# Kernel optimization log

Measured on AMD Instinct MI355X. Metric: run time of the kernel, lower is better.

## Reference

```python
import jax, jax.numpy as jnp
import numpy as np

B, N, D_MODEL, H, DK, DV = 2, 2048, 512, 8, 64, 64


def setup_inputs() -> dict:
    key = jax.random.key(0)
    ks = jax.random.split(key, 15)
    s = 0.02
    f = jnp.float32
    inp = {
        "x": jax.random.normal(ks[0], (B, N, D_MODEL), f),
        # frozen base projections
        "Wq": jax.random.normal(ks[1], (D_MODEL, H * DK), f) * s,
        "bq": jax.random.normal(ks[2], (H * DK,), f) * s,
        "Wk": jax.random.normal(ks[3], (D_MODEL, H * DK), f) * s,
        "bk": jax.random.normal(ks[4], (H * DK,), f) * s,
        "Wv": jax.random.normal(ks[5], (D_MODEL, H * DV), f) * s,
        "bv": jax.random.normal(ks[6], (H * DV,), f) * s,
        # 'lora' adapters (full linears in the source, added to base)
        "Wq_lora": jax.random.normal(ks[7], (D_MODEL, H * DK), f) * s,
        "bq_lora": jax.random.normal(ks[8], (H * DK,), f) * s,
        "Wk_lora": jax.random.normal(ks[9], (D_MODEL, H * DK), f) * s,
        "bk_lora": jax.random.normal(ks[10], (H * DK,), f) * s,
        "Wv_lora": jax.random.normal(ks[11], (D_MODEL, H * DV), f) * s,
        "bv_lora": jax.random.normal(ks[12], (H * DV,), f) * s,
        # output projection
        "Wo": jax.random.normal(ks[13], (H * DV, D_MODEL), f) * s,
        "bo": jax.random.normal(ks[14], (D_MODEL,), f) * s,
    }
    return inp


def reference(x, Wq, bq, Wk, bk, Wv, bv,
              Wq_lora, bq_lora, Wk_lora, bk_lora, Wv_lora, bv_lora,
              Wo, bo):
    b, n, _ = x.shape
    # base + lora pairs share the same input -> fuse into single GEMMs
    q = x @ (Wq + Wq_lora) + (bq + bq_lora)          # [b, n, H*DK]
    k = x @ (Wk + Wk_lora) + (bk + bk_lora)          # [b, n, H*DK]
    v = x @ (Wv + Wv_lora) + (bv + bv_lora)          # [b, n, H*DV]

    q = q.reshape(b, n, H, DK).transpose(0, 2, 1, 3)  # [b, H, n, DK]
    k = k.reshape(b, n, H, DK).transpose(0, 2, 1, 3)
    v = v.reshape(b, n, H, DV).transpose(0, 2, 1, 3)

    scale = 1.0 / jnp.sqrt(jnp.asarray(DK, x.dtype))
    scores = jnp.einsum('bhqd,bhkd->bhqk', q, k) * scale  # [b, H, n, n]
    att = jax.nn.softmax(scores, axis=-1)                 # attn dropout = eval identity
    out = jnp.einsum('bhqk,bhkd->bhqd', att, v)           # [b, H, n, DV]
    out = out.transpose(0, 2, 1, 3).reshape(b, n, H * DV)
    return out @ Wo + bo                                  # resid dropout = eval identity
```

## Files before the change

kernel.cpp:

```cpp
#include <hip/hip_runtime.h>
#include <hip/hip_bf16.h>

#define B_  2
#define N_  2048
#define DM_ 512
#define H_  8
#define DK_ 64
#define DV_ 64
#define BN_ (B_*N_)
#define SPLITS 2

typedef __attribute__((ext_vector_type(8))) short short8;
typedef __attribute__((ext_vector_type(4))) float f32x4;
typedef unsigned short ushort;
typedef __attribute__((address_space(3))) unsigned int lds_u32_t;
typedef const __attribute__((address_space(1))) unsigned int glb_u32_t;

static __device__ __forceinline__ ushort f2bf(float x) {
    unsigned int u = __float_as_uint(x);
    unsigned int r = (u + 0x7FFFu + ((u >> 16) & 1u)) >> 16;
    return (ushort)r;
}
static __device__ __forceinline__ float bf2f(ushort u) {
    return __uint_as_float(((unsigned)u) << 16);
}
static __device__ __forceinline__ float exp2_fast(float x) {
    float r; asm("v_exp_f32 %0, %1" : "=v"(r) : "v"(x)); return r;
}
static __device__ __forceinline__ unsigned cvt_pk_bf16(float a, float b) {
    unsigned r; asm("v_cvt_pk_bf16_f32 %0, %1, %2" : "=v"(r) : "v"(a), "v"(b)); return r;
}

#define LOG2E 1.4426950408889634f

__global__ __launch_bounds__(256) void prep(
        const float* __restrict__ W0, const float* __restrict__ L0,
        const float* __restrict__ W1, const float* __restrict__ L1,
        const float* __restrict__ W2, const float* __restrict__ L2,
        const float* __restrict__ W3, ushort* __restrict__ WtBase,
        const float* __restrict__ x, ushort* __restrict__ xb,
        const float* __restrict__ bq, const float* __restrict__ bqL,
        const float* __restrict__ bk, const float* __restrict__ bkL,
        const float* __restrict__ bv, const float* __restrict__ bvL,
        float* __restrict__ fb) {
    const int bid = blockIdx.x;
    const int t = threadIdx.x;
    if (bid < 512) {
        const int z = bid >> 7, rem = bid & 127;
        const int c0 = (rem & 7) * 64, k0 = (rem >> 3) * 32;
        const float* W  = (z == 0) ? W0 : (z == 1) ? W1 : (z == 2) ? W2 : W3;
        const float* WL = (z == 0) ? L0 : (z == 1) ? L1 : (z == 2) ? L2 : nullptr;
        ushort* Wt = WtBase + (size_t)z * DM_ * DM_;
        __shared__ float Ws[32][65];
        {
            int r = t >> 4, cq = t & 15;
#pragma unroll
            for (int it = 0; it < 2; ++it) {
                int rr = r + it * 16;
                float4 v = *reinterpret_cast<const float4*>(W + (size_t)(k0 + rr) * DM_ + c0 + cq * 4);
                if (WL) {
                    float4 u = *reinterpret_cast<const float4*>(WL + (size_t)(k0 + rr) * DM_ + c0 + cq * 4);
                    v.x += u.x; v.y += u.y; v.z += u.z; v.w += u.w;
                }
                Ws[rr][cq * 4 + 0] = v.x; Ws[rr][cq * 4 + 1] = v.y;
                Ws[rr][cq * 4 + 2] = v.z; Ws[rr][cq * 4 + 3] = v.w;
            }
        }
        __syncthreads();
        {
            int cr = t >> 2, kq = t & 3;
            short8 o;
#pragma unroll
            for (int j = 0; j < 8; ++j) o[j] = (short)f2bf(Ws[kq * 8 + j][cr]);
            *reinterpret_cast<short8*>(Wt + (size_t)(c0 + cr) * DM_ + k0 + kq * 8) = o;
        }
    } else if (bid < 1536) {
        size_t idx = (size_t)(bid - 512) * 256 + t;
        float4 v0 = *reinterpret_cast<const float4*>(x + idx * 8);
        float4 v1 = *reinterpret_cast<const float4*>(x + idx * 8 + 4);
        short8 o;
        o[0] = (short)f2bf(v0.x); o[1] = (short)f2bf(v0.y);
        o[2] = (short)f2bf(v0.z); o[3] = (short)f2bf(v0.w);
        o[4] = (short)f2bf(v1.x); o[5] = (short)f2bf(v1.y);
        o[6] = (short)f2bf(v1.z); o[7] = (short)f2bf(v1.w);
        *reinterpret_cast<short8*>(xb + idx * 8) = o;
    } else {
        int idx = (bid - 1536) * 256 + t;
        if (idx < 3 * DM_) {
            int w = idx >> 9, i = idx & 511;
            const float* a = (w == 0) ? bq : (w == 1) ? bk : bv;
            const float* b = (w == 0) ? bqL : (w == 1) ? bkL : bvL;
            fb[idx] = a[i] + b[i];
        }
    }
}

template<int BN, int MODE>
__global__ __launch_bounds__(256) void gemm_bf16(const ushort* __restrict__ A,
                                                 const ushort* __restrict__ Bt,
                                                 const float* __restrict__ bias,
                                                 ushort* __restrict__ Qd,
                                                 ushort* __restrict__ Kd,
                                                 ushort* __restrict__ Vd,
                                                 float* __restrict__ outF) {
    constexpr int NWC = BN / 64;
    constexpr int NWR = 4 / NWC;
    constexpr int MI  = (128 / NWR) / 16;
    constexpr int NJ  = 4;
    constexpr int BIT = BN / 32;
    const int rt = blockIdx.x, ct = blockIdx.y;
    __shared__ ushort As[2][128 * 64];
    __shared__ ushort Bs[2][BN * 64];
    const int t = threadIdx.x, lane = t & 63, w = t >> 6;
    const int wr = w / NWC, wc = w % NWC;
    const int lg = lane >> 4, lr = lane & 15;
    const int rowbase = wr * (128 / NWR);
    const int colbase = wc * 64;

    f32x4 acc[MI][NJ];
#pragma unroll
    for (int mi = 0; mi < MI; ++mi)
#pragma unroll
        for (int nj = 0; nj < NJ; ++nj) acc[mi][nj] = (f32x4){0.f, 0.f, 0.f, 0.f};

    auto stage = [&](int buf, int k0) {
#pragma unroll
        for (int it = 0; it < 4; ++it) {
            int c = it * 256 + t;
            int r = c >> 3, cq = c & 7;
            int gq = cq ^ (r & 7);
            __builtin_amdgcn_global_load_lds(
                (glb_u32_t*)(A + ((size_t)(rt * 128 + r)) * DM_ + k0 + gq * 8),
                (lds_u32_t*)((char*)(As[buf]) + c * 16), 16, 0, 0);
        }
#pragma unroll
        for (int it = 0; it < BIT; ++it) {
            int c = it * 256 + t;
            int r = c >> 3, cq = c & 7;
            int gq = cq ^ (r & 7);
            __builtin_amdgcn_global_load_lds(
                (glb_u32_t*)(Bt + ((size_t)(ct * BN + r)) * DM_ + k0 + gq * 8),
                (lds_u32_t*)((char*)(Bs[buf]) + c * 16), 16, 0, 0);
        }
    };

    stage(0, 0);
    __syncthreads();

    for (int k0 = 0; k0 < DM_; k0 += 64) {
        const int cur = (k0 >> 6) & 1;
        if (k0 + 64 < DM_) stage(cur ^ 1, k0 + 64);
#pragma unroll
        for (int kh = 0; kh < 2; ++kh) {
            short8 a[MI], b[NJ];
#pragma unroll
            for (int mi = 0; mi < MI; ++mi) {
                int row = rowbase + mi * 16 + lr;
                a[mi] = *reinterpret_cast<const short8*>(
                    (char*)(As[cur]) + row * 128 + (((kh * 4 + lg) ^ (row & 7)) << 4));
            }
#pragma unroll
            for (int nj = 0; nj < NJ; ++nj) {
                int row = colbase + nj * 16 + lr;
                b[nj] = *reinterpret_cast<const short8*>(
                    (char*)(Bs[cur]) + row * 128 + (((kh * 4 + lg) ^ (row & 7)) << 4));
            }
#pragma unroll
            for (int mi = 0; mi < MI; ++mi)
#pragma unroll
                for (int nj = 0; nj < NJ; ++nj)
                    acc[mi][nj] = __builtin_amdgcn_mfma_f32_16x16x32_bf16(
                        a[mi], b[nj], acc[mi][nj], 0, 0, 0);
        }
        __syncthreads();
    }

#pragma unroll
    for (int mi = 0; mi < MI; ++mi) {
#pragma unroll
        for (int nj = 0; nj < NJ; ++nj) {
#pragma unroll
            for (int r = 0; r < 4; ++r) {
                int m = rt * 128 + rowbase + mi * 16 + 4 * lg + r;
                int n = ct * BN + colbase + nj * 16 + lr;
                float v = acc[mi][nj][r] + bias[n];
                if (MODE == 0) {
                    int ws_ = n >> 9;
                    if (ws_ == 0) v *= 0.125f * LOG2E;
                    ushort* op = (ws_ == 0) ? Qd : (ws_ == 1) ? Kd : Vd;
                    int hd = (n >> 6) & 7, d = n & 63;
                    int bb = m >> 11, nn = m & (N_ - 1);
                    op[(((size_t)(bb * H_ + hd)) * N_ + nn) * DK_ + d] = f2bf(v);
                } else {
                    outF[(size_t)m * DM_ + n] = v;
                }
            }
        }
    }
}

__global__ __launch_bounds__(256) void vtrans(const ushort* __restrict__ Vd,
                                              ushort* __restrict__ Vt) {
    const int bh = blockIdx.y, nt = blockIdx.x;
    __shared__ ushort Ls[64 * 64];
    char* LB = (char*)Ls;
    const int t = threadIdx.x;
#pragma unroll
    for (int i = 0; i < 2; ++i) {
        int c = t + i * 256;
        int tok = c >> 3, dc = c & 7;
        uint4 v = *reinterpret_cast<const uint4*>(
            Vd + ((size_t)bh * N_ + nt * 64 + tok) * DV_ + dc * 8);
        int sw = dc ^ (tok & 7) ^ ((tok >> 3) & 7);
        *reinterpret_cast<uint4*>(LB + tok * 128 + (sw << 4)) = v;
    }
    __syncthreads();
#pragma unroll
    for (int i = 0; i < 2; ++i) {
        int c = t + i * 256;
        int d = c >> 3, tc = c & 7;
        short8 g;
#pragma unroll
        for (int j = 0; j < 8; ++j) {
            int tok = tc * 8 + j;
            int sw = (d >> 3) ^ (tok & 7) ^ ((tok >> 3) & 7);
            g[j] = *reinterpret_cast<const ushort*>(LB + tok * 128 + (sw << 4) + (d & 7) * 2);
        }
        *reinterpret_cast<short8*>(Vt + ((size_t)bh * DV_ + d) * N_ + nt * 64 + tc * 8) = g;
    }
}

__global__ __launch_bounds__(512) void attn_mfma(const ushort* __restrict__ Q,
                                                 const ushort* __restrict__ K,
                                                 const ushort* __restrict__ Vt,
                                                 ushort* __restrict__ Opart,
                                                 float2* __restrict__ Ml) {
    const int bh = blockIdx.y;
    const int qt = blockIdx.x;
    const int sp = blockIdx.z;
    const int t  = threadIdx.x;
    const int lane = t & 63;
    const int w  = t >> 6;
    const int lg = lane >> 4;
    const int lr = lane & 15;

    __shared__ ushort KsBuf[2][64 * 64];
    __shared__ ushort VtBuf[2][64 * 64];
    __shared__ ushort Ps[8][16 * 64];
    char* PsB = (char*)(Ps[w]);

    const ushort* Kb  = K  + ((size_t)bh * N_ + sp * (N_ / 2)) * DK_;
    const ushort* Vtb = Vt + (size_t)bh * DV_ * N_ + sp * (N_ / 2);

    const int srow = t >> 3, sc = t & 7;

    short8 qf[2];
    {
        const ushort* qrow = Q + ((size_t)bh * N_ + qt * 128 + w * 16 + lr) * DK_;
        qf[0] = *reinterpret_cast<const short8*>(qrow + 8 * lg);
        qf[1] = *reinterpret_cast<const short8*>(qrow + 32 + 8 * lg);
    }

    f32x4 o_[4];
#pragma unroll
    for (int i = 0; i < 4; i++) o_[i] = (f32x4){0.f, 0.f, 0.f, 0.f};
    float m1 = -1e30f, l1 = 0.f;

    uint4 kreg, vreg;
    auto issue = [&](int kt_) {
        kreg = *reinterpret_cast<const uint4*>(Kb  + ((size_t)(kt_ * 64 + srow)) * DK_ + sc * 8);
        vreg = *reinterpret_cast<const uint4*>(Vtb + (size_t)srow * N_ + kt_ * 64 + sc * 8);
    };
    auto wstage = [&](int buf_) {
        *reinterpret_cast<uint4*>((char*)(KsBuf[buf_]) + srow * 128 + ((sc ^ (srow & 7)) << 4)) = kreg;
        *reinterpret_cast<uint4*>((char*)(VtBuf[buf_]) + srow * 128 + ((sc ^ (srow & 7)) << 4)) = vreg;
    };

    issue(0);
    wstage(0);
    __syncthreads();

    const int NT = (N_ / 2) / 64;
    for (int kt = 0; kt < NT; ++kt) {
        const int cur = kt & 1;
        if (kt + 1 < NT) issue(kt + 1);

        char* KsB = (char*)(KsBuf[cur]);
        char* VtB = (char*)(VtBuf[cur]);

        f32x4 s[4];
#pragma unroll
        for (int kb = 0; kb < 4; ++kb) {
            int row = kb * 16 + lr;
            short8 k0 = *reinterpret_cast<const short8*>(
                KsB + row * 128 + ((lg ^ (row & 7)) << 4));
            short8 k1 = *reinterpret_cast<const short8*>(
                KsB + row * 128 + (((4 + lg) ^ (row & 7)) << 4));
            f32x4 z = (f32x4){0.f, 0.f, 0.f, 0.f};
            s[kb] = __builtin_amdgcn_mfma_f32_16x16x32_bf16(k0, qf[0], z, 0, 0, 0);
            s[kb] = __builtin_amdgcn_mfma_f32_16x16x32_bf16(k1, qf[1], s[kb], 0, 0, 0);
        }

        float mx = s[0][0];
#pragma unroll
        for (int kb = 0; kb < 4; ++kb)
#pragma unroll
            for (int r = 0; r < 4; ++r) mx = fmaxf(mx, s[kb][r]);
        mx = fmaxf(mx, __shfl_xor(mx, 16));
        mx = fmaxf(mx, __shfl_xor(mx, 32));

        if (!__all(mx <= m1 + 8.0f)) {
            float mnew = fmaxf(m1, mx);
            float alpha = exp2_fast(m1 - mnew);
            m1 = mnew;
            l1 *= alpha;
#pragma unroll
            for (int r = 0; r < 4; ++r) {
                float ar = __shfl(alpha, 4 * lg + r);
#pragma unroll
                for (int db = 0; db < 4; ++db) o_[db][r] *= ar;
            }
        }

        float p[4][4];
        float sum = 0.f;
#pragma unroll
        for (int kb = 0; kb < 4; ++kb)
#pragma unroll
            for (int r = 0; r < 4; ++r) { p[kb][r] = exp2_fast(s[kb][r] - m1); sum += p[kb][r]; }
        sum += __shfl_xor(sum, 16);
        sum += __shfl_xor(sum, 32);
        l1 += sum;

#pragma unroll
        for (int kb = 0; kb < 4; ++kb) {
            uint2 pk;
            pk.x = cvt_pk_bf16(p[kb][0], p[kb][1]);
            pk.y = cvt_pk_bf16(p[kb][2], p[kb][3]);
            int chunk = 2 * kb + (lg >> 1);
            *reinterpret_cast<uint2*>(
                PsB + lr * 128 + ((chunk ^ (lr & 7)) << 4) + (lg & 1) * 8) = pk;
        }

        short8 pf[2];
        {
            pf[0] = *reinterpret_cast<const short8*>(
                PsB + lr * 128 + ((lg ^ (lr & 7)) << 4));
            pf[1] = *reinterpret_cast<const short8*>(
                PsB + lr * 128 + (((4 + lg) ^ (lr & 7)) << 4));
        }
#pragma unroll
        for (int db = 0; db < 4; ++db) {
            int row = db * 16 + lr;
            short8 v0 = *reinterpret_cast<const short8*>(
                VtB + row * 128 + ((lg ^ (row & 7)) << 4));
            short8 v1 = *reinterpret_cast<const short8*>(
                VtB + row * 128 + (((4 + lg) ^ (row & 7)) << 4));
            o_[db] = __builtin_amdgcn_mfma_f32_16x16x32_bf16(pf[0], v0, o_[db], 0, 0, 0);
            o_[db] = __builtin_amdgcn_mfma_f32_16x16x32_bf16(pf[1], v1, o_[db], 0, 0, 0);
        }

        if (kt + 1 < NT) wstage(cur ^ 1);
        __syncthreads();
    }

    const size_t rowbase = ((size_t)(sp * 16 + bh)) * N_ + qt * 128 + w * 16;
#pragma unroll
    for (int r = 0; r < 4; ++r) {
        int n_loc = 4 * lg + r;
#pragma unroll
        for (int db = 0; db < 4; ++db) {
            Opart[(rowbase + n_loc) * DV_ + db * 16 + lr] = f2bf(o_[db][r]);
        }
    }
    if (lg == 0) {
        Ml[rowbase + lr] = make_float2(m1, l1);
    }
}

__global__ __launch_bounds__(256) void merge_splits(const ushort* __restrict__ Opart,
                                                    const float2* __restrict__ Ml,
                                                    ushort* __restrict__ Od) {
    int gid = blockIdx.x * 256 + threadIdx.x;
    int row = gid >> 4;
    int dv  = (gid & 15) * 4;
    const int R = 16 * N_;
    float2 ml0 = Ml[row];
    float2 ml1 = Ml[R + row];
    float M  = fmaxf(ml0.x, ml1.x);
    float w0 = exp2_fast(ml0.x - M);
    float w1 = exp2_fast(ml1.x - M);
    float inv = 1.f / (w0 * ml0.y + w1 * ml1.y);
    uint2 a = *reinterpret_cast<const uint2*>(Opart + (size_t)row * DV_ + dv);
    uint2 b = *reinterpret_cast<const uint2*>(Opart + ((size_t)R + row) * DV_ + dv);
    const ushort* ae = reinterpret_cast<const ushort*>(&a);
    const ushort* be = reinterpret_cast<const ushort*>(&b);
    uint2 o;
    unsigned* oe = reinterpret_cast<unsigned*>(&o);
#pragma unroll
    for (int half = 0; half < 2; ++half) {
        float v0 = (w0 * bf2f(ae[half * 2 + 0]) + w1 * bf2f(be[half * 2 + 0])) * inv;
        float v1 = (w0 * bf2f(ae[half * 2 + 1]) + w1 * bf2f(be[half * 2 + 1])) * inv;
        oe[half] = cvt_pk_bf16(v0, v1);
    }
    int bh = row >> 11, n = row & (N_ - 1);
    int bb = bh >> 3, h = bh & 7;
    *reinterpret_cast<uint2*>(Od + ((size_t)(bb * N_ + n)) * (H_ * DV_) + h * DV_ + dv) = o;
}

extern "C" void kernel_launch(void* const* d_in, const int* in_sizes, int n_in,
                              void* d_out, int out_size, void* d_ws, size_t ws_size,
                              hipStream_t stream) {
    const float* x   = (const float*)d_in[0];
    const float* Wq  = (const float*)d_in[1];
    const float* bq  = (const float*)d_in[2];
    const float* Wk  = (const float*)d_in[3];
    const float* bk  = (const float*)d_in[4];
    const float* Wv  = (const float*)d_in[5];
    const float* bv  = (const float*)d_in[6];
    const float* WqL = (const float*)d_in[7];
    const float* bqL = (const float*)d_in[8];
    const float* WkL = (const float*)d_in[9];
    const float* bkL = (const float*)d_in[10];
    const float* WvL = (const float*)d_in[11];
    const float* bvL = (const float*)d_in[12];
    const float* Wo  = (const float*)d_in[13];
    const float* bo  = (const float*)d_in[14];

    ushort* Wt_all = (ushort*)d_ws;
    ushort* Wot    = Wt_all + (size_t)3 * DM_ * DM_;
    float*  fb     = (float*)(Wt_all + (size_t)4 * DM_ * DM_);
    ushort* xbf    = (ushort*)(fb + 3 * DM_);
    ushort* Qd     = xbf + (size_t)BN_ * DM_;
    ushort* Kd     = Qd + (size_t)B_ * H_ * N_ * DK_;
    ushort* Vd     = Kd + (size_t)B_ * H_ * N_ * DK_;
    ushort* Vtd    = Vd + (size_t)B_ * H_ * N_ * DV_;
    ushort* Od     = Vtd + (size_t)B_ * H_ * N_ * DV_;
    ushort* Opart  = Od + (size_t)B_ * H_ * N_ * DV_;
    float2* Ml     = (float2*)(Opart + (size_t)SPLITS * B_ * H_ * N_ * DV_);

    float* out = (float*)d_out;

    prep<<<1542, 256, 0, stream>>>(Wq, WqL, Wk, WkL, Wv, WvL, Wo, Wt_all,
                                   x, xbf, bq, bqL, bk, bkL, bv, bvL, fb);

    gemm_bf16<128, 0><<<dim3(32, 12), 256, 0, stream>>>(xbf, Wt_all, fb, Qd, Kd, Vd, nullptr);
    vtrans<<<dim3(32, 16), 256, 0, stream>>>(Vd, Vtd);
    attn_mfma<<<dim3(16, 16, SPLITS), 512, 0, stream>>>(Qd, Kd, Vtd, Opart, Ml);
    merge_splits<<<(B_ * H_ * N_ * 16) / 256, 256, 0, stream>>>(Opart, Ml, Od);
    gemm_bf16<64, 1><<<dim3(32, 8), 256, 0, stream>>>(Od, Wot, bo, nullptr, nullptr, nullptr, out);
}
```

Measured before the change: 72.28 us.

## Fuse V transpose into QKV GEMM epilogue and raise attention splits to four

The QKV GEMM epilogue now writes V straight into the transposed [bh, d, n] layout as packed bf16 quads, so the separate vtrans kernel and the intermediate V buffer are gone. Attention splits along the key dimension go from 2 to 4, doubling the attention grid to 1024 blocks for better CU occupancy, and merge_splits is generalised to combine any number of partials. The cost is twice as much partial-output and max/sum traffic plus a heavier merge, and the transposed V stores from the GEMM are 8-byte scattered writes.

```diff
diff --git a/kernel.cpp b/kernel.cpp
--- a/kernel.cpp
+++ b/kernel.cpp
@@ -8,7 +8,7 @@
 #define DK_ 64
 #define DV_ 64
 #define BN_ (B_*N_)
-#define SPLITS 2
+#define SPLITS 4
 
 typedef __attribute__((ext_vector_type(8))) short short8;
 typedef __attribute__((ext_vector_type(4))) float f32x4;
@@ -101,7 +101,7 @@
                                                  const float* __restrict__ bias,
                                                  ushort* __restrict__ Qd,
                                                  ushort* __restrict__ Kd,
-                                                 ushort* __restrict__ Vd,
+                                                 ushort* __restrict__ Vtd,
                                                  float* __restrict__ outF) {
     constexpr int NWC = BN / 64;
     constexpr int NWR = 4 / NWC;
@@ -179,54 +179,37 @@
     for (int mi = 0; mi < MI; ++mi) {
 #pragma unroll
         for (int nj = 0; nj < NJ; ++nj) {
-#pragma unroll
-            for (int r = 0; r < 4; ++r) {
-                int m = rt * 128 + rowbase + mi * 16 + 4 * lg + r;
-                int n = ct * BN + colbase + nj * 16 + lr;
-                float v = acc[mi][nj][r] + bias[n];
-                if (MODE == 0) {
-                    int ws_ = n >> 9;
+            int n = ct * BN + colbase + nj * 16 + lr;
+            int m0 = rt * 128 + rowbase + mi * 16 + 4 * lg;
+            if (MODE == 1) {
+#pragma unroll
+                for (int r = 0; r < 4; ++r)
+                    outF[(size_t)(m0 + r) * DM_ + n] = acc[mi][nj][r] + bias[n];
+            } else {
+                int ws_ = n >> 9;
+                float vv[4];
+#pragma unroll
+                for (int r = 0; r < 4; ++r) {
+                    float v = acc[mi][nj][r] + bias[n];
                     if (ws_ == 0) v *= 0.125f * LOG2E;
-                    ushort* op = (ws_ == 0) ? Qd : (ws_ == 1) ? Kd : Vd;
-                    int hd = (n >> 6) & 7, d = n & 63;
-                    int bb = m >> 11, nn = m & (N_ - 1);
-                    op[(((size_t)(bb * H_ + hd)) * N_ + nn) * DK_ + d] = f2bf(v);
+                    vv[r] = v;
+                }
+                int hd = (n >> 6) & 7, d = n & 63;
+                int bb = m0 >> 11, nn = m0 & (N_ - 1);
+                if (ws_ < 2) {
+                    ushort* op = (ws_ == 0) ? Qd : Kd;
+#pragma unroll
+                    for (int r = 0; r < 4; ++r)
+                        op[(((size_t)(bb * H_ + hd)) * N_ + nn + r) * DK_ + d] = f2bf(vv[r]);
                 } else {
-                    outF[(size_t)m * DM_ + n] = v;
+                    uint2 pk;
+                    pk.x = cvt_pk_bf16(vv[0], vv[1]);
+                    pk.y = cvt_pk_bf16(vv[2], vv[3]);
+                    *reinterpret_cast<uint2*>(
+                        Vtd + (((size_t)(bb * H_ + hd)) * DV_ + d) * N_ + nn) = pk;
                 }
             }
         }
-    }
-}
-
-__global__ __launch_bounds__(256) void vtrans(const ushort* __restrict__ Vd,
-                                              ushort* __restrict__ Vt) {
-    const int bh = blockIdx.y, nt = blockIdx.x;
-    __shared__ ushort Ls[64 * 64];
-    char* LB = (char*)Ls;
-    const int t = threadIdx.x;
-#pragma unroll
-    for (int i = 0; i < 2; ++i) {
-        int c = t + i * 256;
-        int tok = c >> 3, dc = c & 7;
-        uint4 v = *reinterpret_cast<const uint4*>(
-            Vd + ((size_t)bh * N_ + nt * 64 + tok) * DV_ + dc * 8);
-        int sw = dc ^ (tok & 7) ^ ((tok >> 3) & 7);
-        *reinterpret_cast<uint4*>(LB + tok * 128 + (sw << 4)) = v;
-    }
-    __syncthreads();
-#pragma unroll
-    for (int i = 0; i < 2; ++i) {
-        int c = t + i * 256;
-        int d = c >> 3, tc = c & 7;
-        short8 g;
-#pragma unroll
-        for (int j = 0; j < 8; ++j) {
-            int tok = tc * 8 + j;
-            int sw = (d >> 3) ^ (tok & 7) ^ ((tok >> 3) & 7);
-            g[j] = *reinterpret_cast<const ushort*>(LB + tok * 128 + (sw << 4) + (d & 7) * 2);
-        }
-        *reinterpret_cast<short8*>(Vt + ((size_t)bh * DV_ + d) * N_ + nt * 64 + tc * 8) = g;
     }
 }
 
@@ -249,8 +232,8 @@
     __shared__ ushort Ps[8][16 * 64];
     char* PsB = (char*)(Ps[w]);
 
-    const ushort* Kb  = K  + ((size_t)bh * N_ + sp * (N_ / 2)) * DK_;
-    const ushort* Vtb = Vt + (size_t)bh * DV_ * N_ + sp * (N_ / 2);
+    const ushort* Kb  = K  + ((size_t)bh * N_ + sp * (N_ / SPLITS)) * DK_;
+    const ushort* Vtb = Vt + (size_t)bh * DV_ * N_ + sp * (N_ / SPLITS);
 
     const int srow = t >> 3, sc = t & 7;
 
@@ -280,7 +263,7 @@
     wstage(0);
     __syncthreads();
 
-    const int NT = (N_ / 2) / 64;
+    const int NT = (N_ / SPLITS) / 64;
     for (int kt = 0; kt < NT; ++kt) {
         const int cur = kt & 1;
         if (kt + 1 < NT) issue(kt + 1);
@@ -385,24 +368,25 @@
     int row = gid >> 4;
     int dv  = (gid & 15) * 4;
     const int R = 16 * N_;
-    float2 ml0 = Ml[row];
-    float2 ml1 = Ml[R + row];
-    float M  = fmaxf(ml0.x, ml1.x);
-    float w0 = exp2_fast(ml0.x - M);
-    float w1 = exp2_fast(ml1.x - M);
-    float inv = 1.f / (w0 * ml0.y + w1 * ml1.y);
-    uint2 a = *reinterpret_cast<const uint2*>(Opart + (size_t)row * DV_ + dv);
-    uint2 b = *reinterpret_cast<const uint2*>(Opart + ((size_t)R + row) * DV_ + dv);
-    const ushort* ae = reinterpret_cast<const ushort*>(&a);
-    const ushort* be = reinterpret_cast<const ushort*>(&b);
+    float2 ml[SPLITS];
+    float M = -1e30f;
+#pragma unroll
+    for (int s = 0; s < SPLITS; ++s) { ml[s] = Ml[(size_t)s * R + row]; M = fmaxf(M, ml[s].x); }
+    float wgt[SPLITS], denom = 0.f;
+#pragma unroll
+    for (int s = 0; s < SPLITS; ++s) { wgt[s] = exp2_fast(ml[s].x - M); denom += wgt[s] * ml[s].y; }
+    float inv = 1.f / denom;
+    float a0 = 0.f, a1 = 0.f, a2 = 0.f, a3 = 0.f;
+#pragma unroll
+    for (int s = 0; s < SPLITS; ++s) {
+        uint2 u = *reinterpret_cast<const uint2*>(Opart + ((size_t)s * R + row) * DV_ + dv);
+        const ushort* e = reinterpret_cast<const ushort*>(&u);
+        a0 += wgt[s] * bf2f(e[0]); a1 += wgt[s] * bf2f(e[1]);
+        a2 += wgt[s] * bf2f(e[2]); a3 += wgt[s] * bf2f(e[3]);
+    }
     uint2 o;
-    unsigned* oe = reinterpret_cast<unsigned*>(&o);
-#pragma unroll
-    for (int half = 0; half < 2; ++half) {
-        float v0 = (w0 * bf2f(ae[half * 2 + 0]) + w1 * bf2f(be[half * 2 + 0])) * inv;
-        float v1 = (w0 * bf2f(ae[half * 2 + 1]) + w1 * bf2f(be[half * 2 + 1])) * inv;
-        oe[half] = cvt_pk_bf16(v0, v1);
-    }
+    o.x = cvt_pk_bf16(a0 * inv, a1 * inv);
+    o.y = cvt_pk_bf16(a2 * inv, a3 * inv);
     int bh = row >> 11, n = row & (N_ - 1);
     int bb = bh >> 3, h = bh & 7;
     *reinterpret_cast<uint2*>(Od + ((size_t)(bb * N_ + n)) * (H_ * DV_) + h * DV_ + dv) = o;
@@ -433,8 +417,7 @@
     ushort* xbf    = (ushort*)(fb + 3 * DM_);
     ushort* Qd     = xbf + (size_t)BN_ * DM_;
     ushort* Kd     = Qd + (size_t)B_ * H_ * N_ * DK_;
-    ushort* Vd     = Kd + (size_t)B_ * H_ * N_ * DK_;
-    ushort* Vtd    = Vd + (size_t)B_ * H_ * N_ * DV_;
+    ushort* Vtd    = Kd + (size_t)B_ * H_ * N_ * DK_;
     ushort* Od     = Vtd + (size_t)B_ * H_ * N_ * DV_;
     ushort* Opart  = Od + (size_t)B_ * H_ * N_ * DV_;
     float2* Ml     = (float2*)(Opart + (size_t)SPLITS * B_ * H_ * N_ * DV_);
@@ -444,8 +427,7 @@
     prep<<<1542, 256, 0, stream>>>(Wq, WqL, Wk, WkL, Wv, WvL, Wo, Wt_all,
                                    x, xbf, bq, bqL, bk, bkL, bv, bvL, fb);
 
-    gemm_bf16<128, 0><<<dim3(32, 12), 256, 0, stream>>>(xbf, Wt_all, fb, Qd, Kd, Vd, nullptr);
-    vtrans<<<dim3(32, 16), 256, 0, stream>>>(Vd, Vtd);
+    gemm_bf16<128, 0><<<dim3(32, 12), 256, 0, stream>>>(xbf, Wt_all, fb, Qd, Kd, Vtd, nullptr);
     attn_mfma<<<dim3(16, 16, SPLITS), 512, 0, stream>>>(Qd, Kd, Vtd, Opart, Ml);
     merge_splits<<<(B_ * H_ * N_ * 16) / 256, 256, 0, stream>>>(Opart, Ml, Od);
     gemm_bf16<64, 1><<<dim3(32, 8), 256, 0, stream>>>(Od, Wot, bo, nullptr, nullptr, nullptr, out);
```

After: 65.72 us. 1.1x faster.
